# Optimization experiments

Hardware: AMD Instinct MI355X
Metric: run time of the kernel (lower is better)

Reference implementation:

```python
import jax, jax.numpy as jnp
import numpy as np
from jax import lax

GAP_PENALTY = 0.0
TEMPERATURE = 1.0
B, A, L, D, K = 64, 26, 384, 512, 18


def setup_inputs() -> dict:
    key = jax.random.key(0)
    k1, k2, k3, k4 = jax.random.split(key, 4)
    matrices = jax.random.normal(k1, (B, A, L), dtype=jnp.float32)
    # ragged lengths: (len_i, len_0) per pair, in [L//2, L]
    shapes = jax.random.randint(k2, (B, 2), L // 2, L + 1, dtype=jnp.int32)
    s = 1.0 / np.sqrt(A * K)  # torch Conv1d default init scale
    conv_w = jax.random.uniform(k3, (D, A, K), minval=-s, maxval=s, dtype=jnp.float32)
    conv_b = jax.random.uniform(k4, (D,), minval=-s, maxval=s, dtype=jnp.float32)
    return {"matrices": matrices, "shapes": shapes, "conv_w": conv_w, "conv_b": conv_b}


def _smoothmax3(a, b, c, t):
    # t * log(exp(a/t) + exp(b/t) + exp(c/t)), numerically stable
    m = jnp.maximum(jnp.maximum(a, b), c)
    return m + t * jnp.log(jnp.exp((a - m) / t) + jnp.exp((b - m) / t) + jnp.exp((c - m) / t))


def _nw_matrix(sim, t, g):
    # sim: (L, L). Returns smoothed NW value matrix V: (L+1, L+1).
    # V[i,j] = sim[i-1,j-1] + smoothmax(V[i-1,j-1], V[i-1,j]-g, V[i,j-1]-g)
    n = sim.shape[0]
    row0 = -g * jnp.arange(n + 1, dtype=sim.dtype)  # free/affine leading gaps on top row

    def row_step(prev_row, inp):
        s_row, i = inp  # s_row: (L,)
        v_left0 = -g * i  # V[i, 0]

        def col_step(left, xs):
            s, diag, up = xs
            v = s + _smoothmax3(diag, up - g, left - g, t)
            return v, v

        _, rest = lax.scan(col_step, v_left0, (s_row, prev_row[:-1], prev_row[1:]))
        new_row = jnp.concatenate([v_left0[None], rest])
        return new_row, new_row

    _, rows = lax.scan(row_step, row0, (sim, jnp.arange(1, n + 1, dtype=sim.dtype)))
    return jnp.concatenate([row0[None], rows], axis=0)


def needleman_wunsch(sim, shapes, gap_penalty, temperature):
    # sim: (B, L, L) similarity vs sequence 0; shapes: (B, 2) int lengths.
    # Soft alignment posterior = grad of smoothed terminal score wrt similarity.
    li = jnp.clip(shapes[:, 0], 0, sim.shape[1])
    lj = jnp.clip(shapes[:, 1], 0, sim.shape[2])

    def total_score(s):
        V = jax.vmap(lambda m: _nw_matrix(m, temperature, gap_penalty))(s)  # (B, L+1, L+1)
        b = jnp.arange(s.shape[0])
        return jnp.sum(V[b, li, lj])

    return jax.grad(total_score)(sim)  # (B, L, L), expected match matrix


def reference(matrices, shapes, conv_w, conv_b):
    # Conv1d padding='same' with even kernel: torch pads (k-1)//2 left, k//2 right
    k = conv_w.shape[-1]
    pad = ((k - 1) // 2, k // 2)
    emb = lax.conv_general_dilated(
        matrices, conv_w, window_strides=(1,), padding=[pad],
        dimension_numbers=("NCH", "OIH", "NCH"),
    ) + conv_b[None, :, None]  # (B, D, L)
    e = jnp.transpose(emb, (0, 2, 1))  # (B, L, D)
    sim = jnp.einsum("bld,md->blm", e, e[0])  # (B, L_i, L_0): similarity vs sequence 0
    align = needleman_wunsch(sim, shapes, GAP_PENALTY, TEMPERATURE)  # (B, L, L)
    m = jnp.transpose(matrices, (0, 2, 1))  # (B, L, A)
    # consensus in sequence-0 coordinates, then project back to each sequence
    consensus = jnp.mean(jnp.einsum("nia,nij->nja", m, align), axis=0)  # (L, A)
    return jnp.einsum("ja,nij->nia", consensus, align)  # (B, L, A)
```

## Files before the change

kernel.cpp:

```cpp
#include <hip/hip_runtime.h>
#include <hip/hip_bf16.h>
#include <math.h>

#define B_  64
#define A_  26
#define L_  384
#define D_  512
#define K_  18
#define KC  480
#define LL  147456
#define SZD 245760

typedef __attribute__((ext_vector_type(8))) short bf16x8;
typedef __attribute__((ext_vector_type(4))) float f32x4;
typedef unsigned short ushort_t;
typedef unsigned int uint_t;

__device__ __forceinline__ void stD(float* sp, int z, int c, float v) {
    int dl = z / 6, dr = z - dl * 6;
    sp[(size_t)(dl + (c >> 2)) * 1536 + dr * 256 + dl * 4 + (c & 3)] = v;
}

__device__ __forceinline__ ushort_t f2bf(float v) {
    uint_t u = __float_as_uint(v);
    uint_t r = (u + 0x7FFFu + ((u >> 16) & 1u)) >> 16;
    return (ushort_t)r;
}

__global__ void wsplit_kernel(const float* __restrict__ w, ushort_t* __restrict__ wh,
                              ushort_t* __restrict__ wl) {
    int o = blockIdx.x * blockDim.x + threadIdx.x;
    if (o >= D_ * KC) return;
    int d = o / KC, r = o - d * KC;
    float v = (r < A_ * K_) ? w[(size_t)d * (A_ * K_) + r] : 0.0f;
    ushort_t h = f2bf(v);
    float hf = __uint_as_float(((uint_t)h) << 16);
    wh[o] = h;
    wl[o] = f2bf(v - hf);
}

__global__ __launch_bounds__(256) void im2col_kernel(const float* __restrict__ x,
                                                     ushort_t* __restrict__ xh,
                                                     ushort_t* __restrict__ xl) {
    int b  = blockIdx.y;
    int lt = blockIdx.x;
    const float* xb = x + (size_t)b * A_ * L_;
    for (int idx = threadIdx.x; idx < 64 * KC; idx += 256) {
        int l = lt * 64 + idx / KC;
        int r = idx % KC;
        float v = 0.0f;
        if (r < A_ * K_) {
            int a = r / K_, kk = r - a * K_;
            int g = l + kk - 8;
            if (g >= 0 && g < L_) v = xb[(size_t)a * L_ + g];
        }
        ushort_t h = f2bf(v);
        float hf = __uint_as_float(((uint_t)h) << 16);
        size_t o = ((size_t)b * L_ + l) * KC + r;
        xh[o] = h;
        xl[o] = f2bf(v - hf);
    }
}

__global__ __launch_bounds__(256) void convmm_kernel(const ushort_t* __restrict__ xh,
                                                     const ushort_t* __restrict__ xl,
                                                     const ushort_t* __restrict__ wh,
                                                     const ushort_t* __restrict__ wl,
                                                     const float* __restrict__ bias,
                                                     ushort_t* __restrict__ ehi,
                                                     ushort_t* __restrict__ elo) {
    int b = blockIdx.z;
    int w = threadIdx.x >> 6;
    int lane = threadIdx.x & 63;
    int l0 = blockIdx.y * 64 + 32 * (w >> 1);
    int d0 = blockIdx.x * 64 + 32 * (w & 1);
    int r = lane & 15, g = lane >> 4;
    const ushort_t* pah = xh + ((size_t)b * L_ + l0 + r) * KC + g * 8;
    const ushort_t* pal = xl + ((size_t)b * L_ + l0 + r) * KC + g * 8;
    const ushort_t* pbh = wh + (size_t)(d0 + r) * KC + g * 8;
    const ushort_t* pbl = wl + (size_t)(d0 + r) * KC + g * 8;
    f32x4 acc00 = {0.f, 0.f, 0.f, 0.f}, acc01 = acc00, acc10 = acc00, acc11 = acc00;
#pragma unroll 3
    for (int ks = 0; ks < 15; ++ks) {
        int off = ks * 32;
        bf16x8 Ah0 = *(const bf16x8*)(pah + off);
        bf16x8 Ah1 = *(const bf16x8*)(pah + 16 * KC + off);
        bf16x8 Al0 = *(const bf16x8*)(pal + off);
        bf16x8 Al1 = *(const bf16x8*)(pal + 16 * KC + off);
        bf16x8 Bh0 = *(const bf16x8*)(pbh + off);
        bf16x8 Bh1 = *(const bf16x8*)(pbh + 16 * KC + off);
        bf16x8 Bl0 = *(const bf16x8*)(pbl + off);
        bf16x8 Bl1 = *(const bf16x8*)(pbl + 16 * KC + off);
        acc00 = __builtin_amdgcn_mfma_f32_16x16x32_bf16(Ah0, Bh0, acc00, 0, 0, 0);
        acc00 = __builtin_amdgcn_mfma_f32_16x16x32_bf16(Ah0, Bl0, acc00, 0, 0, 0);
        acc00 = __builtin_amdgcn_mfma_f32_16x16x32_bf16(Al0, Bh0, acc00, 0, 0, 0);
        acc01 = __builtin_amdgcn_mfma_f32_16x16x32_bf16(Ah0, Bh1, acc01, 0, 0, 0);
        acc01 = __builtin_amdgcn_mfma_f32_16x16x32_bf16(Ah0, Bl1, acc01, 0, 0, 0);
        acc01 = __builtin_amdgcn_mfma_f32_16x16x32_bf16(Al0, Bh1, acc01, 0, 0, 0);
        acc10 = __builtin_amdgcn_mfma_f32_16x16x32_bf16(Ah1, Bh0, acc10, 0, 0, 0);
        acc10 = __builtin_amdgcn_mfma_f32_16x16x32_bf16(Ah1, Bl0, acc10, 0, 0, 0);
        acc10 = __builtin_amdgcn_mfma_f32_16x16x32_bf16(Al1, Bh0, acc10, 0, 0, 0);
        acc11 = __builtin_amdgcn_mfma_f32_16x16x32_bf16(Ah1, Bh1, acc11, 0, 0, 0);
        acc11 = __builtin_amdgcn_mfma_f32_16x16x32_bf16(Ah1, Bl1, acc11, 0, 0, 0);
        acc11 = __builtin_amdgcn_mfma_f32_16x16x32_bf16(Al1, Bh1, acc11, 0, 0, 0);
    }
#pragma unroll
    for (int v = 0; v < 4; ++v) {
        int lr0 = l0 + g * 4 + v, lr1 = lr0 + 16;
        int dc0 = d0 + r,         dc1 = dc0 + 16;
        float vals[4] = {acc00[v] + bias[dc0], acc01[v] + bias[dc1],
                         acc10[v] + bias[dc0], acc11[v] + bias[dc1]};
        int lrs[4] = {lr0, lr0, lr1, lr1};
        int dcs[4] = {dc0, dc1, dc0, dc1};
#pragma unroll
        for (int t = 0; t < 4; ++t) {
            ushort_t h = f2bf(vals[t]);
            float hf = __uint_as_float(((uint_t)h) << 16);
            size_t o = ((size_t)b * L_ + lrs[t]) * D_ + dcs[t];
            ehi[o] = h;
            elo[o] = f2bf(vals[t] - hf);
        }
    }
}

__global__ __launch_bounds__(256) void sim_kernel(const ushort_t* __restrict__ ehi,
                                                  const ushort_t* __restrict__ elo,
                                                  float* __restrict__ simD) {
    int b = blockIdx.z;
    int w = threadIdx.x >> 6;
    int lane = threadIdx.x & 63;
    int l0 = blockIdx.y * 64 + 32 * (w >> 1);
    int m0 = blockIdx.x * 64 + 32 * (w & 1);
    int r = lane & 15, g = lane >> 4;
    size_t rowA = ((size_t)b * L_ + l0 + r) * D_ + g * 8;
    size_t rowB = ((size_t)m0 + r) * D_ + g * 8;
    const ushort_t* pah = ehi + rowA;
    const ushort_t* pal = elo + rowA;
    const ushort_t* pbh = ehi + rowB;
    const ushort_t* pbl = elo + rowB;
    f32x4 acc00 = {0.f, 0.f, 0.f, 0.f}, acc01 = acc00, acc10 = acc00, acc11 = acc00;
#pragma unroll 2
    for (int ks = 0; ks < 16; ++ks) {
        int off = ks * 32;
        bf16x8 Ah0 = *(const bf16x8*)(pah + off);
        bf16x8 Ah1 = *(const bf16x8*)(pah + 16 * D_ + off);
        bf16x8 Al0 = *(const bf16x8*)(pal + off);
        bf16x8 Al1 = *(const bf16x8*)(pal + 16 * D_ + off);
        bf16x8 Bh0 = *(const bf16x8*)(pbh + off);
        bf16x8 Bh1 = *(const bf16x8*)(pbh + 16 * D_ + off);
        bf16x8 Bl0 = *(const bf16x8*)(pbl + off);
        bf16x8 Bl1 = *(const bf16x8*)(pbl + 16 * D_ + off);
        acc00 = __builtin_amdgcn_mfma_f32_16x16x32_bf16(Ah0, Bh0, acc00, 0, 0, 0);
        acc00 = __builtin_amdgcn_mfma_f32_16x16x32_bf16(Ah0, Bl0, acc00, 0, 0, 0);
        acc00 = __builtin_amdgcn_mfma_f32_16x16x32_bf16(Al0, Bh0, acc00, 0, 0, 0);
        acc01 = __builtin_amdgcn_mfma_f32_16x16x32_bf16(Ah0, Bh1, acc01, 0, 0, 0);
        acc01 = __builtin_amdgcn_mfma_f32_16x16x32_bf16(Ah0, Bl1, acc01, 0, 0, 0);
        acc01 = __builtin_amdgcn_mfma_f32_16x16x32_bf16(Al0, Bh1, acc01, 0, 0, 0);
        acc10 = __builtin_amdgcn_mfma_f32_16x16x32_bf16(Ah1, Bh0, acc10, 0, 0, 0);
        acc10 = __builtin_amdgcn_mfma_f32_16x16x32_bf16(Ah1, Bl0, acc10, 0, 0, 0);
        acc10 = __builtin_amdgcn_mfma_f32_16x16x32_bf16(Al1, Bh0, acc10, 0, 0, 0);
        acc11 = __builtin_amdgcn_mfma_f32_16x16x32_bf16(Ah1, Bh1, acc11, 0, 0, 0);
        acc11 = __builtin_amdgcn_mfma_f32_16x16x32_bf16(Ah1, Bl1, acc11, 0, 0, 0);
        acc11 = __builtin_amdgcn_mfma_f32_16x16x32_bf16(Al1, Bh1, acc11, 0, 0, 0);
    }
    float* sp = simD + (size_t)b * SZD;
#pragma unroll
    for (int v = 0; v < 4; ++v) {
        int ar0 = l0 + g * 4 + v, ar1 = ar0 + 16;
        int ac0 = m0 + r,         ac1 = ac0 + 16;
        stD(sp, ar0, ac0, acc00[v]);
        stD(sp, ar0, ac1, acc01[v]);
        stD(sp, ar1, ac0, acc10[v]);
        stD(sp, ar1, ac1, acc11[v]);
    }
}

__global__ __launch_bounds__(256, 1) void nw_fwd_kernel(const float* __restrict__ simD, float* __restrict__ VD) {
    int b = blockIdx.x;
    int tid = threadIdx.x;
    int w = tid >> 6, l = tid & 63;
    __shared__ float4 MA[4][64], MB4[4][64], MC[4][64];
    __shared__ int FL[4];
    const float4 Z4 = {0.f, 0.f, 0.f, 0.f};
    for (int k = tid; k < 256; k += 256) {
        int s = k >> 6, ll = k & 63;
        MA[s][ll] = Z4; MB4[s][ll] = Z4; MC[s][ll] = Z4;
    }
    if (tid < 4) FL[tid] = (tid == 3) ? -1 : -1000000;
    __syncthreads();
    volatile int* flg = FL;
    const float* pS = simD + (size_t)b * SZD + l * 4;
    float*       pV = VD   + (size_t)b * SZD + l * 4;
    float4 buf[6];
#pragma unroll
    for (int r = 0; r < 6; ++r) buf[r] = *(const float4*)(pS + w * 1536 + r * 256);
    int lm = (l == 0) ? 0 : (l - 1);
#pragma unroll 1
    for (int T = w; T < 159; T += 4) {
        int sp = (T - 1) & 3;
        while (flg[sp] != T - 1) {}
        asm volatile("" ::: "memory");
        float4 Ar = MA[sp][l];
        float4 Bs = MB4[sp][l];
        float4 Cs = MC[sp][l];
        float4 Bn = MB4[sp][lm];
        float4 Cn = MC[sp][lm];
        if (l == 0) { Bn = Z4; Cn = Z4; }
        float vleft[6] = {Ar.x, Ar.y, Ar.z, Ar.w, Bs.x, Bs.y};
        float d0 = Bn.z;
        float uin[4] = {Cn.x, Cn.y, Cn.z, Cn.w};
        float sc[6][4];
#pragma unroll
        for (int r = 0; r < 6; ++r) {
            sc[r][0] = buf[r].x; sc[r][1] = buf[r].y; sc[r][2] = buf[r].z; sc[r][3] = buf[r].w;
        }
        int dP = min(T + 4, 158);
#pragma unroll
        for (int r = 0; r < 6; ++r) buf[r] = *(const float4*)(pS + dP * 1536 + r * 256);
        int ct = T - l;
        float nbc[4] = {0.f, 0.f, 0.f, 0.f}, nbp = 0.f;
        if (ct >= 0 && ct <= 95) {
            float vout[6][4];
#pragma unroll
            for (int q = 0; q < 4; ++q) {
                float dg = (q == 0) ? d0 : uin[q - 1];
                float up = uin[q];
#pragma unroll
                for (int r = 0; r < 6; ++r) {
                    float lf = vleft[r];
                    float mx = fmaxf(dg, fmaxf(up, lf));
                    float v = sc[r][q] + mx + __logf(__expf(dg - mx) + __expf(up - mx) + __expf(lf - mx));
                    dg = lf; up = v;
                    vleft[r] = v;
                    vout[r][q] = v;
                }
            }
            nbp = Cs.w;
#pragma unroll
            for (int q = 0; q < 4; ++q) nbc[q] = vout[5][q];
            float* pVd = pV + (size_t)T * 1536;
#pragma unroll
            for (int r = 0; r < 6; ++r) {
                float4 t;
                t.x = vout[r][0]; t.y = vout[r][1]; t.z = vout[r][2]; t.w = vout[r][3];
                *(float4*)(pVd + r * 256) = t;
            }
        }
        float4 pa; pa.x = vleft[0]; pa.y = vleft[1]; pa.z = vleft[2]; pa.w = vleft[3];
        float4 pb; pb.x = vleft[4]; pb.y = vleft[5]; pb.z = nbp; pb.w = 0.f;
        float4 pc; pc.x = nbc[0]; pc.y = nbc[1]; pc.z = nbc[2]; pc.w = nbc[3];
        MA[w][l] = pa; MB4[w][l] = pb; MC[w][l] = pc;
        asm volatile("s_waitcnt lgkmcnt(0)" ::: "memory");
        if (l == 0) flg[w] = T;
    }
}

__global__ __launch_bounds__(256, 1) void nw_bwd_kernel(const float* __restrict__ simD,
                                                        const float* __restrict__ VD,
                                                        const int* __restrict__ shapes,
                                                        float* __restrict__ ED) {
    int b = blockIdx.x;
    int tid = threadIdx.x;
    int w = tid >> 6, l = tid & 63;
    __shared__ float4 MA[4][64], MB4[4][64], MC[4][64], MD[4][64], MEx[4][64], MF[4][64];
    __shared__ int FL[4];
    const float4 Z4 = {0.f, 0.f, 0.f, 0.f};
    for (int k = tid; k < 256; k += 256) {
        int s = k >> 6, ll = k & 63;
        MA[s][ll] = Z4; MB4[s][ll] = Z4; MC[s][ll] = Z4;
        MD[s][ll] = Z4; MEx[s][ll] = Z4; MF[s][ll] = Z4;
    }
    if (tid < 4) FL[tid] = (tid == 3) ? -1 : -1000000;
    __syncthreads();
    volatile int* flg = FL;
    const float* pS = simD + (size_t)b * SZD + l * 4;
    const float* pV = VD   + (size_t)b * SZD + l * 4;
    float*       pE = ED   + (size_t)b * SZD + l * 4;
    int li = min(max(shapes[2 * b + 0], 0), L_);
    int lj = min(max(shapes[2 * b + 1], 0), L_);
    float4 bufV[6], bufS[6];
#pragma unroll
    for (int r = 0; r < 6; ++r) {
        bufV[r] = *(const float4*)(pV + (158 - w) * 1536 + r * 256);
        bufS[r] = *(const float4*)(pS + (158 - w) * 1536 + r * 256);
    }
    int lp = (l == 63) ? 63 : (l + 1);
#pragma unroll 1
    for (int T = w; T < 159; T += 4) {
        int sp = (T - 1) & 3;
        while (flg[sp] != T - 1) {}
        asm volatile("" ::: "memory");
        float4 Ar = MA[sp][l];
        float4 Br = MB4[sp][l];
        float4 Cr = MC[sp][l];
        float4 Dn = MD[sp][lp];
        float4 En = MEx[sp][lp];
        float4 Fn = MF[sp][lp];
        if (l == 63) { Dn = Z4; En = Z4; Fn = Z4; }
        float e[6] = {Ar.x, Ar.y, Ar.z, Ar.w, Br.x, Br.y};
        float u[6] = {Br.z, Br.w, Cr.x, Cr.y, Cr.z, Cr.w};
        float enb_c[4] = {Dn.x, Dn.y, Dn.z, Dn.w};
        float unb_c[4] = {En.x, En.y, En.z, En.w};
        float enbtd_s = Fn.x, unbtd_s = Fn.y;
        float e0r = e[0], u0r = u[0];
        float Vq[6][4], Sq[6][4];
#pragma unroll
        for (int r = 0; r < 6; ++r) {
            Vq[r][0] = bufV[r].x; Vq[r][1] = bufV[r].y; Vq[r][2] = bufV[r].z; Vq[r][3] = bufV[r].w;
            Sq[r][0] = bufS[r].x; Sq[r][1] = bufS[r].y; Sq[r][2] = bufS[r].z; Sq[r][3] = bufS[r].w;
        }
        int dP = max(158 - (T + 4), 0);
#pragma unroll
        for (int r = 0; r < 6; ++r) {
            bufV[r] = *(const float4*)(pV + dP * 1536 + r * 256);
            bufS[r] = *(const float4*)(pS + dP * 1536 + r * 256);
        }
        int ct = 158 - T - l;
        float necar[4] = {0.f, 0.f, 0.f, 0.f}, nucar[4] = {0.f, 0.f, 0.f, 0.f};
        if (ct >= 0 && ct <= 95) {
            float Eo[6][4];
#pragma unroll
            for (int qq = 0; qq < 4; ++qq) {
                const int q = 3 - qq;
                int j = 4 * ct + q + 1;
                bool jlt = (j < L_);
                float eo[6], uo[6];
#pragma unroll
                for (int r = 0; r < 6; ++r) { eo[r] = e[r]; uo[r] = u[r]; }
#pragma unroll
                for (int rr = 0; rr < 6; ++rr) {
                    const int r = 5 - rr;
                    int i = 6 * l + r + 1;
                    bool ilt = (i < L_);
                    float Vv = Vq[r][q];
                    float u_new = Vv - Sq[r][q];
                    float eb_old, ub_old, eb_new, ub_new;
                    if (r == 5) {
                        eb_old = (q == 3) ? enbtd_s : enb_c[q + 1];
                        ub_old = (q == 3) ? unbtd_s : unb_c[q + 1];
                        eb_new = enb_c[q];
                        ub_new = unb_c[q];
                    } else {
                        eb_old = eo[r + 1]; ub_old = uo[r + 1];
                        eb_new = e[r + 1];  ub_new = u[r + 1];
                    }
                    float wtd = (ilt && jlt) ? __expf(Vv - ub_old) : 0.f;
                    float wtu = ilt ? __expf(Vv - ub_new) : 0.f;
                    float wtl = jlt ? __expf(Vv - uo[r]) : 0.f;
                    float en = (i == li && j == lj) ? 1.f : 0.f;
                    en += wtd * eb_old + wtu * eb_new + wtl * eo[r];
                    e[r] = en; u[r] = u_new;
                    Eo[r][q] = en;
                }
            }
#pragma unroll
            for (int q = 0; q < 4; ++q) {
                necar[q] = Eo[0][q];
                nucar[q] = Vq[0][q] - Sq[0][q];
            }
            float* pEd = pE + (size_t)(158 - T) * 1536;
#pragma unroll
            for (int r = 0; r < 6; ++r) {
                float4 t;
                t.x = Eo[r][0]; t.y = Eo[r][1]; t.z = Eo[r][2]; t.w = Eo[r][3];
                *(float4*)(pEd + r * 256) = t;
            }
        }
        float4 pa; pa.x = e[0]; pa.y = e[1]; pa.z = e[2]; pa.w = e[3];
        float4 pb; pb.x = e[4]; pb.y = e[5]; pb.z = u[0]; pb.w = u[1];
        float4 pc; pc.x = u[2]; pc.y = u[3]; pc.z = u[4]; pc.w = u[5];
        float4 pd; pd.x = necar[0]; pd.y = necar[1]; pd.z = necar[2]; pd.w = necar[3];
        float4 pe; pe.x = nucar[0]; pe.y = nucar[1]; pe.z = nucar[2]; pe.w = nucar[3];
        float4 pf; pf.x = e0r; pf.y = u0r; pf.z = 0.f; pf.w = 0.f;
        MA[w][l] = pa; MB4[w][l] = pb; MC[w][l] = pc;
        MD[w][l] = pd; MEx[w][l] = pe; MF[w][l] = pf;
        asm volatile("s_waitcnt lgkmcnt(0)" ::: "memory");
        if (l == 0) flg[w] = T;
    }
}

__global__ __launch_bounds__(256) void repack_kernel(const float* __restrict__ ED,
                                                     float* __restrict__ Enat) {
    int n  = blockIdx.y;
    int jt = blockIdx.x;
    int jl = threadIdx.x & 63;
    int gp = threadIdx.x >> 6;
    int j  = jt * 64 + jl;
    const float* eb = ED + (size_t)n * SZD + (j >> 2) * 1536 + (j & 3);
    float* ob = Enat + (size_t)n * LL + j;
#pragma unroll 4
    for (int i = gp * 96; i < gp * 96 + 96; ++i) {
        int dl = i / 6, dr = i - dl * 6;
        float v = eb[(size_t)dl * 1540 + dr * 256];
        ob[(size_t)i * L_] = v;
    }
}

__global__ __launch_bounds__(256) void consensus_kernel(const float* __restrict__ x,
                                                        const float* __restrict__ Enat,
                                                        float* __restrict__ cons) {
    int n  = blockIdx.y;
    int j0 = blockIdx.x * 64;
    __shared__ float ms[A_][L_];
    for (int idx = threadIdx.x; idx < A_ * L_; idx += 256)
        ((float*)ms)[idx] = x[(size_t)n * A_ * L_ + idx];
    __syncthreads();
    int jl = threadIdx.x & 63;
    int g  = threadIdx.x >> 6;
    int a0 = g * 7;
    int na = (a0 + 7 <= A_) ? 7 : (A_ - a0);
    int j  = j0 + jl;
    float acc[7] = {0.f, 0.f, 0.f, 0.f, 0.f, 0.f, 0.f};
    const float* aE = Enat + (size_t)n * LL + j;
    for (int i = 0; i < L_; ++i) {
        float al = aE[(size_t)i * L_];
#pragma unroll
        for (int t = 0; t < 7; ++t)
            if (t < na) acc[t] = fmaf(al, ms[a0 + t][i], acc[t]);
    }
    for (int t = 0; t < na; ++t)
        atomicAdd(&cons[(size_t)j * A_ + a0 + t], acc[t] * (1.0f / B_));
}

__global__ __launch_bounds__(256) void out_kernel(const float* __restrict__ Enat,
                                                  const float* __restrict__ cons,
                                                  float* __restrict__ out) {
    int n  = blockIdx.y;
    int i0 = blockIdx.x * 32;
    __shared__ float cs[L_][A_];
    __shared__ float as_[32][L_ + 1];
    for (int idx = threadIdx.x; idx < L_ * A_; idx += 256)
        ((float*)cs)[idx] = cons[idx];
    const float* aE = Enat + (size_t)n * LL;
    for (int idx = threadIdx.x; idx < 32 * L_; idx += 256) {
        int r = idx / L_, c = idx - r * L_;
        as_[r][c] = aE[(size_t)(i0 + r) * L_ + c];
    }
    __syncthreads();
    for (int o = threadIdx.x; o < 32 * A_; o += 256) {
        int il = o / A_, a = o % A_;
        float s = 0.f;
        for (int jj = 0; jj < L_; ++jj)
            s = fmaf(as_[il][jj], cs[jj][a], s);
        out[((size_t)n * L_ + i0 + il) * A_ + a] = s;
    }
}

extern "C" void kernel_launch(void* const* d_in, const int* in_sizes, int n_in,
                              void* d_out, int out_size, void* d_ws, size_t ws_size,
                              hipStream_t stream) {
    const float* matrices = (const float*)d_in[0];
    const int*   shapes   = (const int*)d_in[1];
    const float* conv_w   = (const float*)d_in[2];
    const float* conv_b   = (const float*)d_in[3];
    float* out = (float*)d_out;

    char* p = (char*)d_ws;
    float*    EDiag = (float*)p;
    ushort_t* xh = (ushort_t*)p;
    ushort_t* xl = xh + (size_t)B_ * L_ * KC;
    p += (size_t)B_ * SZD * 4;
    ushort_t* ehi = (ushort_t*)p;
    ushort_t* elo = ehi + (size_t)B_ * L_ * D_;
    p += (size_t)B_ * L_ * D_ * 4;
    float* simD = (float*)p;
    float* Enat = simD;
    p += (size_t)B_ * SZD * 4;
    float* VD = (float*)p;
    p += (size_t)B_ * SZD * 4;
    ushort_t* wh = (ushort_t*)p;
    ushort_t* wl = wh + (size_t)D_ * KC;
    p += (size_t)D_ * KC * 4;
    float* cons = (float*)p;

    wsplit_kernel<<<(D_ * KC + 255) / 256, 256, 0, stream>>>(conv_w, wh, wl);
    im2col_kernel<<<dim3(L_ / 64, B_), 256, 0, stream>>>(matrices, xh, xl);
    convmm_kernel<<<dim3(D_ / 64, L_ / 64, B_), 256, 0, stream>>>(xh, xl, wh, wl, conv_b, ehi, elo);
    sim_kernel<<<dim3(L_ / 64, L_ / 64, B_), 256, 0, stream>>>(ehi, elo, simD);
    nw_fwd_kernel<<<B_, 256, 0, stream>>>(simD, VD);
    nw_bwd_kernel<<<B_, 256, 0, stream>>>(simD, VD, shapes, EDiag);
    repack_kernel<<<dim3(L_ / 64, B_), 256, 0, stream>>>(EDiag, Enat);
    hipMemsetAsync(cons, 0, (size_t)L_ * A_ * sizeof(float), stream);
    consensus_kernel<<<dim3(L_ / 64, B_), 256, 0, stream>>>(matrices, Enat, cons);
    out_kernel<<<dim3(L_ / 32, B_), 256, 0, stream>>>(Enat, cons, out);
}
```

Before: 1.017 ms.

## Tile GEMM operands into K-chunked layout and wavefront-order NW cell updates

Stores the im2col, weight and embedding hi/lo bf16 buffers in a blocked layout of 32-element K chunks, so each MFMA fragment load reads contiguous 64-byte rows instead of strided rows with a large pitch. The NW forward and backward per-thread 6x4 tile updates are reordered along anti-diagonals, and the backward pass precomputes all exp weights before the dependent recurrence. This exposes independent exp/log work to the scheduler and shortens the serial dependency chain. It raises register pressure from the extra per-cell arrays.

```diff
diff --git a/kernel.cpp b/kernel.cpp
--- a/kernel.cpp
+++ b/kernel.cpp
@@ -35,8 +35,9 @@
     float v = (r < A_ * K_) ? w[(size_t)d * (A_ * K_) + r] : 0.0f;
     ushort_t h = f2bf(v);
     float hf = __uint_as_float(((uint_t)h) << 16);
-    wh[o] = h;
-    wl[o] = f2bf(v - hf);
+    size_t oo = ((size_t)(r >> 5) * D_ + d) * 32 + (r & 31);
+    wh[oo] = h;
+    wl[oo] = f2bf(v - hf);
 }
 
 __global__ __launch_bounds__(256) void im2col_kernel(const float* __restrict__ x,
@@ -56,7 +57,7 @@
         }
         ushort_t h = f2bf(v);
         float hf = __uint_as_float(((uint_t)h) << 16);
-        size_t o = ((size_t)b * L_ + l) * KC + r;
+        size_t o = (((size_t)b * 15 + (r >> 5)) * L_ + l) * 32 + (r & 31);
         xh[o] = h;
         xl[o] = f2bf(v - hf);
     }
@@ -75,22 +76,23 @@
     int l0 = blockIdx.y * 64 + 32 * (w >> 1);
     int d0 = blockIdx.x * 64 + 32 * (w & 1);
     int r = lane & 15, g = lane >> 4;
-    const ushort_t* pah = xh + ((size_t)b * L_ + l0 + r) * KC + g * 8;
-    const ushort_t* pal = xl + ((size_t)b * L_ + l0 + r) * KC + g * 8;
-    const ushort_t* pbh = wh + (size_t)(d0 + r) * KC + g * 8;
-    const ushort_t* pbl = wl + (size_t)(d0 + r) * KC + g * 8;
+    const ushort_t* pah = xh + (((size_t)b * 15) * L_ + l0 + r) * 32 + g * 8;
+    const ushort_t* pal = xl + (((size_t)b * 15) * L_ + l0 + r) * 32 + g * 8;
+    const ushort_t* pbh = wh + (size_t)(d0 + r) * 32 + g * 8;
+    const ushort_t* pbl = wl + (size_t)(d0 + r) * 32 + g * 8;
     f32x4 acc00 = {0.f, 0.f, 0.f, 0.f}, acc01 = acc00, acc10 = acc00, acc11 = acc00;
 #pragma unroll 3
     for (int ks = 0; ks < 15; ++ks) {
-        int off = ks * 32;
-        bf16x8 Ah0 = *(const bf16x8*)(pah + off);
-        bf16x8 Ah1 = *(const bf16x8*)(pah + 16 * KC + off);
-        bf16x8 Al0 = *(const bf16x8*)(pal + off);
-        bf16x8 Al1 = *(const bf16x8*)(pal + 16 * KC + off);
-        bf16x8 Bh0 = *(const bf16x8*)(pbh + off);
-        bf16x8 Bh1 = *(const bf16x8*)(pbh + 16 * KC + off);
-        bf16x8 Bl0 = *(const bf16x8*)(pbl + off);
-        bf16x8 Bl1 = *(const bf16x8*)(pbl + 16 * KC + off);
+        size_t offA = (size_t)ks * L_ * 32;
+        size_t offB = (size_t)ks * D_ * 32;
+        bf16x8 Ah0 = *(const bf16x8*)(pah + offA);
+        bf16x8 Ah1 = *(const bf16x8*)(pah + offA + 16 * 32);
+        bf16x8 Al0 = *(const bf16x8*)(pal + offA);
+        bf16x8 Al1 = *(const bf16x8*)(pal + offA + 16 * 32);
+        bf16x8 Bh0 = *(const bf16x8*)(pbh + offB);
+        bf16x8 Bh1 = *(const bf16x8*)(pbh + offB + 16 * 32);
+        bf16x8 Bl0 = *(const bf16x8*)(pbl + offB);
+        bf16x8 Bl1 = *(const bf16x8*)(pbl + offB + 16 * 32);
         acc00 = __builtin_amdgcn_mfma_f32_16x16x32_bf16(Ah0, Bh0, acc00, 0, 0, 0);
         acc00 = __builtin_amdgcn_mfma_f32_16x16x32_bf16(Ah0, Bl0, acc00, 0, 0, 0);
         acc00 = __builtin_amdgcn_mfma_f32_16x16x32_bf16(Al0, Bh0, acc00, 0, 0, 0);
@@ -116,7 +118,7 @@
         for (int t = 0; t < 4; ++t) {
             ushort_t h = f2bf(vals[t]);
             float hf = __uint_as_float(((uint_t)h) << 16);
-            size_t o = ((size_t)b * L_ + lrs[t]) * D_ + dcs[t];
+            size_t o = (((size_t)b * 16 + (dcs[t] >> 5)) * L_ + lrs[t]) * 32 + (dcs[t] & 31);
             ehi[o] = h;
             elo[o] = f2bf(vals[t] - hf);
         }
@@ -132,24 +134,22 @@
     int l0 = blockIdx.y * 64 + 32 * (w >> 1);
     int m0 = blockIdx.x * 64 + 32 * (w & 1);
     int r = lane & 15, g = lane >> 4;
-    size_t rowA = ((size_t)b * L_ + l0 + r) * D_ + g * 8;
-    size_t rowB = ((size_t)m0 + r) * D_ + g * 8;
-    const ushort_t* pah = ehi + rowA;
-    const ushort_t* pal = elo + rowA;
-    const ushort_t* pbh = ehi + rowB;
-    const ushort_t* pbl = elo + rowB;
+    const ushort_t* pah = ehi + (((size_t)b * 16) * L_ + l0 + r) * 32 + g * 8;
+    const ushort_t* pal = elo + (((size_t)b * 16) * L_ + l0 + r) * 32 + g * 8;
+    const ushort_t* pbh = ehi + ((size_t)(m0 + r)) * 32 + g * 8;
+    const ushort_t* pbl = elo + ((size_t)(m0 + r)) * 32 + g * 8;
     f32x4 acc00 = {0.f, 0.f, 0.f, 0.f}, acc01 = acc00, acc10 = acc00, acc11 = acc00;
 #pragma unroll 2
     for (int ks = 0; ks < 16; ++ks) {
-        int off = ks * 32;
+        size_t off = (size_t)ks * L_ * 32;
         bf16x8 Ah0 = *(const bf16x8*)(pah + off);
-        bf16x8 Ah1 = *(const bf16x8*)(pah + 16 * D_ + off);
+        bf16x8 Ah1 = *(const bf16x8*)(pah + off + 16 * 32);
         bf16x8 Al0 = *(const bf16x8*)(pal + off);
-        bf16x8 Al1 = *(const bf16x8*)(pal + 16 * D_ + off);
+        bf16x8 Al1 = *(const bf16x8*)(pal + off + 16 * 32);
         bf16x8 Bh0 = *(const bf16x8*)(pbh + off);
-        bf16x8 Bh1 = *(const bf16x8*)(pbh + 16 * D_ + off);
+        bf16x8 Bh1 = *(const bf16x8*)(pbh + off + 16 * 32);
         bf16x8 Bl0 = *(const bf16x8*)(pbl + off);
-        bf16x8 Bl1 = *(const bf16x8*)(pbl + 16 * D_ + off);
+        bf16x8 Bl1 = *(const bf16x8*)(pbl + off + 16 * 32);
         acc00 = __builtin_amdgcn_mfma_f32_16x16x32_bf16(Ah0, Bh0, acc00, 0, 0, 0);
         acc00 = __builtin_amdgcn_mfma_f32_16x16x32_bf16(Ah0, Bl0, acc00, 0, 0, 0);
         acc00 = __builtin_amdgcn_mfma_f32_16x16x32_bf16(Al0, Bh0, acc00, 0, 0, 0);
@@ -182,8 +182,8 @@
     __shared__ float4 MA[4][64], MB4[4][64], MC[4][64];
     __shared__ int FL[4];
     const float4 Z4 = {0.f, 0.f, 0.f, 0.f};
-    for (int k = tid; k < 256; k += 256) {
-        int s = k >> 6, ll = k & 63;
+    {
+        int s = tid >> 6, ll = tid & 63;
         MA[s][ll] = Z4; MB4[s][ll] = Z4; MC[s][ll] = Z4;
     }
     if (tid < 4) FL[tid] = (tid == 3) ? -1 : -1000000;
@@ -222,22 +222,25 @@
         if (ct >= 0 && ct <= 95) {
             float vout[6][4];
 #pragma unroll
-            for (int q = 0; q < 4; ++q) {
-                float dg = (q == 0) ? d0 : uin[q - 1];
-                float up = uin[q];
+            for (int dd = 0; dd < 9; ++dd) {
 #pragma unroll
                 for (int r = 0; r < 6; ++r) {
-                    float lf = vleft[r];
+                    const int q = dd - r;
+                    if (q < 0 || q > 3) continue;
+                    float dg = (r == 0) ? ((q == 0) ? d0 : uin[q - 1])
+                                        : ((q == 0) ? vleft[r - 1] : vout[r - 1][q - 1]);
+                    float up = (r == 0) ? uin[q] : vout[r - 1][q];
+                    float lf = (q == 0) ? vleft[r] : vout[r][q - 1];
                     float mx = fmaxf(dg, fmaxf(up, lf));
-                    float v = sc[r][q] + mx + __logf(__expf(dg - mx) + __expf(up - mx) + __expf(lf - mx));
-                    dg = lf; up = v;
-                    vleft[r] = v;
-                    vout[r][q] = v;
+                    vout[r][q] = sc[r][q] + mx +
+                        __logf(__expf(dg - mx) + __expf(up - mx) + __expf(lf - mx));
                 }
             }
             nbp = Cs.w;
 #pragma unroll
             for (int q = 0; q < 4; ++q) nbc[q] = vout[5][q];
+#pragma unroll
+            for (int r = 0; r < 6; ++r) vleft[r] = vout[r][3];
             float* pVd = pV + (size_t)T * 1536;
 #pragma unroll
             for (int r = 0; r < 6; ++r) {
@@ -265,8 +268,8 @@
     __shared__ float4 MA[4][64], MB4[4][64], MC[4][64], MD[4][64], MEx[4][64], MF[4][64];
     __shared__ int FL[4];
     const float4 Z4 = {0.f, 0.f, 0.f, 0.f};
-    for (int k = tid; k < 256; k += 256) {
-        int s = k >> 6, ll = k & 63;
+    {
+        int s = tid >> 6, ll = tid & 63;
         MA[s][ll] = Z4; MB4[s][ll] = Z4; MC[s][ll] = Z4;
         MD[s][ll] = Z4; MEx[s][ll] = Z4; MF[s][ll] = Z4;
     }
@@ -297,12 +300,11 @@
         float4 En = MEx[sp][lp];
         float4 Fn = MF[sp][lp];
         if (l == 63) { Dn = Z4; En = Z4; Fn = Z4; }
-        float e[6] = {Ar.x, Ar.y, Ar.z, Ar.w, Br.x, Br.y};
-        float u[6] = {Br.z, Br.w, Cr.x, Cr.y, Cr.z, Cr.w};
+        float einit[6] = {Ar.x, Ar.y, Ar.z, Ar.w, Br.x, Br.y};
+        float uinit[6] = {Br.z, Br.w, Cr.x, Cr.y, Cr.z, Cr.w};
         float enb_c[4] = {Dn.x, Dn.y, Dn.z, Dn.w};
         float unb_c[4] = {En.x, En.y, En.z, En.w};
         float enbtd_s = Fn.x, unbtd_s = Fn.y;
-        float e0r = e[0], u0r = u[0];
         float Vq[6][4], Sq[6][4];
 #pragma unroll
         for (int r = 0; r < 6; ++r) {
@@ -317,47 +319,56 @@
         }
         int ct = 158 - T - l;
         float necar[4] = {0.f, 0.f, 0.f, 0.f}, nucar[4] = {0.f, 0.f, 0.f, 0.f};
+        float eC[6], uC[6];
+#pragma unroll
+        for (int r = 0; r < 6; ++r) { eC[r] = einit[r]; uC[r] = uinit[r]; }
         if (ct >= 0 && ct <= 95) {
+            float Uo[6][4];
+#pragma unroll
+            for (int r = 0; r < 6; ++r)
+#pragma unroll
+                for (int q = 0; q < 4; ++q)
+                    Uo[r][q] = Vq[r][q] - Sq[r][q];
+            float wtd[6][4], wtu[6][4], wtl[6][4];
+#pragma unroll
+            for (int r = 0; r < 6; ++r) {
+                int i = 6 * l + r + 1;
+                bool ilt = (i < L_);
+#pragma unroll
+                for (int q = 0; q < 4; ++q) {
+                    int j = 4 * ct + q + 1;
+                    bool jlt = (j < L_);
+                    float ub_old = (r == 5) ? ((q == 3) ? unbtd_s : unb_c[q + 1])
+                                            : ((q == 3) ? uinit[r + 1] : Uo[r + 1][q + 1]);
+                    float ub_new = (r == 5) ? unb_c[q] : Uo[r + 1][q];
+                    float uo_r   = (q == 3) ? uinit[r] : Uo[r][q + 1];
+                    wtd[r][q] = (ilt && jlt) ? __expf(Vq[r][q] - ub_old) : 0.f;
+                    wtu[r][q] = ilt ? __expf(Vq[r][q] - ub_new) : 0.f;
+                    wtl[r][q] = jlt ? __expf(Vq[r][q] - uo_r) : 0.f;
+                }
+            }
             float Eo[6][4];
 #pragma unroll
-            for (int qq = 0; qq < 4; ++qq) {
-                const int q = 3 - qq;
-                int j = 4 * ct + q + 1;
-                bool jlt = (j < L_);
-                float eo[6], uo[6];
-#pragma unroll
-                for (int r = 0; r < 6; ++r) { eo[r] = e[r]; uo[r] = u[r]; }
-#pragma unroll
-                for (int rr = 0; rr < 6; ++rr) {
-                    const int r = 5 - rr;
+            for (int dd = 0; dd < 9; ++dd) {
+#pragma unroll
+                for (int r = 5; r >= 0; --r) {
+                    const int q = 8 - dd - r;
+                    if (q < 0 || q > 3) continue;
                     int i = 6 * l + r + 1;
-                    bool ilt = (i < L_);
-                    float Vv = Vq[r][q];
-                    float u_new = Vv - Sq[r][q];
-                    float eb_old, ub_old, eb_new, ub_new;
-                    if (r == 5) {
-                        eb_old = (q == 3) ? enbtd_s : enb_c[q + 1];
-                        ub_old = (q == 3) ? unbtd_s : unb_c[q + 1];
-                        eb_new = enb_c[q];
-                        ub_new = unb_c[q];
-                    } else {
-                        eb_old = eo[r + 1]; ub_old = uo[r + 1];
-                        eb_new = e[r + 1];  ub_new = u[r + 1];
-                    }
-                    float wtd = (ilt && jlt) ? __expf(Vv - ub_old) : 0.f;
-                    float wtu = ilt ? __expf(Vv - ub_new) : 0.f;
-                    float wtl = jlt ? __expf(Vv - uo[r]) : 0.f;
+                    int j = 4 * ct + q + 1;
+                    float eb_old = (r == 5) ? ((q == 3) ? enbtd_s : enb_c[q + 1])
+                                            : ((q == 3) ? einit[r + 1] : Eo[r + 1][q + 1]);
+                    float eb_new = (r == 5) ? enb_c[q] : Eo[r + 1][q];
+                    float eo_r   = (q == 3) ? einit[r] : Eo[r][q + 1];
                     float en = (i == li && j == lj) ? 1.f : 0.f;
-                    en += wtd * eb_old + wtu * eb_new + wtl * eo[r];
-                    e[r] = en; u[r] = u_new;
+                    en += wtd[r][q] * eb_old + wtu[r][q] * eb_new + wtl[r][q] * eo_r;
                     Eo[r][q] = en;
                 }
             }
 #pragma unroll
-            for (int q = 0; q < 4; ++q) {
-                necar[q] = Eo[0][q];
-                nucar[q] = Vq[0][q] - Sq[0][q];
-            }
+            for (int r = 0; r < 6; ++r) { eC[r] = Eo[r][0]; uC[r] = Uo[r][0]; }
+#pragma unroll
+            for (int q = 0; q < 4; ++q) { necar[q] = Eo[0][q]; nucar[q] = Uo[0][q]; }
             float* pEd = pE + (size_t)(158 - T) * 1536;
 #pragma unroll
             for (int r = 0; r < 6; ++r) {
@@ -366,12 +377,12 @@
                 *(float4*)(pEd + r * 256) = t;
             }
         }
-        float4 pa; pa.x = e[0]; pa.y = e[1]; pa.z = e[2]; pa.w = e[3];
-        float4 pb; pb.x = e[4]; pb.y = e[5]; pb.z = u[0]; pb.w = u[1];
-        float4 pc; pc.x = u[2]; pc.y = u[3]; pc.z = u[4]; pc.w = u[5];
+        float4 pa; pa.x = eC[0]; pa.y = eC[1]; pa.z = eC[2]; pa.w = eC[3];
+        float4 pb; pb.x = eC[4]; pb.y = eC[5]; pb.z = uC[0]; pb.w = uC[1];
+        float4 pc; pc.x = uC[2]; pc.y = uC[3]; pc.z = uC[4]; pc.w = uC[5];
         float4 pd; pd.x = necar[0]; pd.y = necar[1]; pd.z = necar[2]; pd.w = necar[3];
         float4 pe; pe.x = nucar[0]; pe.y = nucar[1]; pe.z = nucar[2]; pe.w = nucar[3];
-        float4 pf; pf.x = e0r; pf.y = u0r; pf.z = 0.f; pf.w = 0.f;
+        float4 pf; pf.x = einit[0]; pf.y = uinit[0]; pf.z = 0.f; pf.w = 0.f;
         MA[w][l] = pa; MB4[w][l] = pb; MC[w][l] = pc;
         MD[w][l] = pd; MEx[w][l] = pe; MF[w][l] = pf;
         asm volatile("s_waitcnt lgkmcnt(0)" ::: "memory");
@@ -458,10 +469,10 @@
     char* p = (char*)d_ws;
     float*    EDiag = (float*)p;
     ushort_t* xh = (ushort_t*)p;
-    ushort_t* xl = xh + (size_t)B_ * L_ * KC;
+    ushort_t* xl = xh + (size_t)B_ * 15 * L_ * 32;
     p += (size_t)B_ * SZD * 4;
     ushort_t* ehi = (ushort_t*)p;
-    ushort_t* elo = ehi + (size_t)B_ * L_ * D_;
+    ushort_t* elo = ehi + (size_t)B_ * 16 * L_ * 32;
     p += (size_t)B_ * L_ * D_ * 4;
     float* simD = (float*)p;
     float* Enat = simD;
@@ -469,8 +480,8 @@
     float* VD = (float*)p;
     p += (size_t)B_ * SZD * 4;
     ushort_t* wh = (ushort_t*)p;
-    ushort_t* wl = wh + (size_t)D_ * KC;
-    p += (size_t)D_ * KC * 4;
+    ushort_t* wl = wh + (size_t)15 * D_ * 32;
+    p += (size_t)15 * D_ * 32 * 4;
     float* cons = (float*)p;
 
     wsplit_kernel<<<(D_ * KC + 255) / 256, 256, 0, stream>>>(conv_w, wh, wl);
```

Result: faster. 941.9 us (-7.4%).
